# Performance work log

Measured on AMD Instinct MI355X. Metric: run time of the kernel, lower is better.

The kernel has to match this reference:

```python
import jax, jax.numpy as jnp
import numpy as np

B, T, C, H = 4, 2048, 1024, 16
D = C // H          # head_dim = 64
FF = 2 * C          # ff_mult = 2
EPS = 1e-5


def _layernorm(x, g, b):
    mu = jnp.mean(x, axis=-1, keepdims=True)
    var = jnp.mean((x - mu) ** 2, axis=-1, keepdims=True)
    return (x - mu) * jax.lax.rsqrt(var + EPS) * g + b


def setup_inputs() -> dict:
    key = jax.random.key(0)
    ks = jax.random.split(key, 8)
    x = jax.random.normal(ks[0], (B, T, C), dtype=jnp.float32)
    perm = jax.random.permutation(ks[1], T).astype(jnp.int32)
    s_c = 1.0 / np.sqrt(C)
    s_f = 1.0 / np.sqrt(FF)
    Wqkv = jax.random.normal(ks[2], (C, 3 * C), dtype=jnp.float32) * s_c
    Wproj = jax.random.normal(ks[3], (C, C), dtype=jnp.float32) * s_c
    bproj = jnp.zeros((C,), dtype=jnp.float32)
    ln1_g = jnp.ones((C,), dtype=jnp.float32)
    ln1_b = jnp.zeros((C,), dtype=jnp.float32)
    ln2_g = jnp.ones((C,), dtype=jnp.float32)
    ln2_b = jnp.zeros((C,), dtype=jnp.float32)
    Wff1 = jax.random.normal(ks[4], (C, FF), dtype=jnp.float32) * s_c
    bff1 = jnp.zeros((FF,), dtype=jnp.float32)
    Wff2 = jax.random.normal(ks[5], (FF, C), dtype=jnp.float32) * s_f
    bff2 = jnp.zeros((C,), dtype=jnp.float32)
    return {"x": x, "perm": perm, "Wqkv": Wqkv, "Wproj": Wproj, "bproj": bproj,
            "ln1_g": ln1_g, "ln1_b": ln1_b, "ln2_g": ln2_g, "ln2_b": ln2_b,
            "Wff1": Wff1, "bff1": bff1, "Wff2": Wff2, "bff2": bff2}


def reference(x, perm, Wqkv, Wproj, bproj, ln1_g, ln1_b, ln2_g, ln2_b,
              Wff1, bff1, Wff2, bff2):
    # --- attention branch ---
    h = _layernorm(x, ln1_g, ln1_b)                       # [B,T,C]
    qkv = (h @ Wqkv).reshape(B, T, 3, H, D)
    q, k, v = qkv[:, :, 0], qkv[:, :, 1], qkv[:, :, 2]    # [B,T,H,D]
    # random-permuted causal additive mask: masked = ~tril[:, perm]
    rows = jnp.arange(T)[:, None]
    masked = perm[None, :] > rows                          # [T,T] bool
    bias = jnp.where(masked, -jnp.inf, 0.0).astype(x.dtype)
    scale = 1.0 / np.sqrt(D)
    scores = jnp.einsum('bqhd,bkhd->bhqk', q, k) * scale + bias
    attn = jax.nn.softmax(scores, axis=-1)                 # [B,H,T,T]
    y = jnp.einsum('bhqk,bkhd->bqhd', attn, v).reshape(B, T, C)
    x = x + y @ Wproj + bproj
    # --- MLP branch ---
    h2 = _layernorm(x, ln2_g, ln2_b)
    ff = jax.nn.gelu(h2 @ Wff1 + bff1, approximate=False) @ Wff2 + bff2
    return x + ff
```

## Files before the change

kernel.cpp:

```cpp
#include <hip/hip_runtime.h>
#include <math.h>

#define Bb 4
#define Tt 2048
#define Cc 1024
#define Hh 16
#define Dd 64
#define FFf 2048
#define Mrows (Bb*Tt)

typedef _Float16 f16;
typedef _Float16 half8 __attribute__((ext_vector_type(8)));
typedef _Float16 half4 __attribute__((ext_vector_type(4)));
typedef _Float16 half2 __attribute__((ext_vector_type(2)));
typedef float floatx4 __attribute__((ext_vector_type(4)));
typedef float floatx16 __attribute__((ext_vector_type(16)));

#define MFMA16(a,b,c)    __builtin_amdgcn_mfma_f32_16x16x32_f16(a,b,c,0,0,0)
#define MFMA16K16(a,b,c) __builtin_amdgcn_mfma_f32_16x16x16f16(a,b,c,0,0,0)
#define MFMA32(a,b,c)    __builtin_amdgcn_mfma_f32_32x32x16_f16(a,b,c,0,0,0)

__device__ __forceinline__ void g2l16(const void* g, void* l) {
  __builtin_amdgcn_global_load_lds((__attribute__((address_space(1))) void*)(g),
                                   (__attribute__((address_space(3))) void*)(l),
                                   16, 0, 0);
}

__global__ __launch_bounds__(256) void wt_ln_kernel(
    const float* __restrict__ Wqkv, const float* __restrict__ Wproj,
    const float* __restrict__ Wff1, const float* __restrict__ Wff2,
    f16* __restrict__ WqkvT, f16* __restrict__ WprojT,
    f16* __restrict__ Wff1T, f16* __restrict__ Wff2T,
    const float* __restrict__ x, const float* __restrict__ gam,
    const float* __restrict__ bet, f16* __restrict__ lnout,
    const int* __restrict__ perm, int* __restrict__ inv) {
  const int tid = threadIdx.x;
  if (blockIdx.x >= 16384) {
    #pragma unroll
    for (int i = tid; i < Tt; i += 256) inv[perm[i]] = i;
    return;
  }
  if (blockIdx.x < 8192) {
    __shared__ float tile[32][33];
    int idx = blockIdx.x;
    const float* W; f16* WT; int K, N, n0, k0;
    if (idx < 3072)      { W = Wqkv;  WT = WqkvT;  K = Cc;  N = 3*Cc; n0 = (idx % 96)*32; k0 = (idx / 96)*32; }
    else if (idx < 4096) { idx -= 3072; W = Wproj; WT = WprojT; K = Cc;  N = Cc;  n0 = (idx % 32)*32; k0 = (idx / 32)*32; }
    else if (idx < 6144) { idx -= 4096; W = Wff1;  WT = Wff1T;  K = Cc;  N = FFf; n0 = (idx % 64)*32; k0 = (idx / 64)*32; }
    else                 { idx -= 6144; W = Wff2;  WT = Wff2T;  K = FFf; N = Cc;  n0 = (idx % 32)*32; k0 = (idx / 32)*32; }
    const int tx = tid & 31, ty = tid >> 5;
    #pragma unroll
    for (int i = 0; i < 4; i++)
      tile[ty + 8*i][tx] = W[(size_t)(k0 + ty + 8*i) * N + n0 + tx];
    __syncthreads();
    #pragma unroll
    for (int i = 0; i < 4; i++)
      WT[(size_t)(n0 + ty + 8*i) * K + k0 + tx] = (f16)tile[tx][ty + 8*i];
  } else {
    const int row = blockIdx.x - 8192;
    const float4 v = ((const float4*)(x + (size_t)row * Cc))[tid];
    float s  = v.x + v.y + v.z + v.w;
    float ss = v.x*v.x + v.y*v.y + v.z*v.z + v.w*v.w;
    #pragma unroll
    for (int o = 32; o >= 1; o >>= 1) { s += __shfl_xor(s, o); ss += __shfl_xor(ss, o); }
    __shared__ float ps[4], pss[4];
    if ((tid & 63) == 0) { ps[tid >> 6] = s; pss[tid >> 6] = ss; }
    __syncthreads();
    s  = ps[0] + ps[1] + ps[2] + ps[3];
    ss = pss[0] + pss[1] + pss[2] + pss[3];
    const float mu   = s * (1.0f / Cc);
    const float rstd = rsqrtf(ss * (1.0f / Cc) - mu * mu + 1e-5f);
    const float4 g4 = ((const float4*)gam)[tid];
    const float4 b4 = ((const float4*)bet)[tid];
    half4 o;
    o[0] = (f16)((v.x - mu) * rstd * g4.x + b4.x);
    o[1] = (f16)((v.y - mu) * rstd * g4.y + b4.y);
    o[2] = (f16)((v.z - mu) * rstd * g4.z + b4.z);
    o[3] = (f16)((v.w - mu) * rstd * g4.w + b4.w);
    ((half4*)(lnout + (size_t)row * Cc))[tid] = o;
  }
}

__global__ __launch_bounds__(256) void ln_kernel(const float* __restrict__ x,
                                                 const float* __restrict__ gam,
                                                 const float* __restrict__ bet,
                                                 f16* __restrict__ out) {
  const int row = blockIdx.x;
  const int tid = threadIdx.x;
  const float4 v = ((const float4*)(x + (size_t)row * Cc))[tid];
  float s  = v.x + v.y + v.z + v.w;
  float ss = v.x*v.x + v.y*v.y + v.z*v.z + v.w*v.w;
  #pragma unroll
  for (int o = 32; o >= 1; o >>= 1) { s += __shfl_xor(s, o); ss += __shfl_xor(ss, o); }
  __shared__ float ps[4], pss[4];
  if ((tid & 63) == 0) { ps[tid >> 6] = s; pss[tid >> 6] = ss; }
  __syncthreads();
  s  = ps[0] + ps[1] + ps[2] + ps[3];
  ss = pss[0] + pss[1] + pss[2] + pss[3];
  const float mu   = s * (1.0f / Cc);
  const float rstd = rsqrtf(ss * (1.0f / Cc) - mu * mu + 1e-5f);
  const float4 g4 = ((const float4*)gam)[tid];
  const float4 b4 = ((const float4*)bet)[tid];
  half4 o;
  o[0] = (f16)((v.x - mu) * rstd * g4.x + b4.x);
  o[1] = (f16)((v.y - mu) * rstd * g4.y + b4.y);
  o[2] = (f16)((v.z - mu) * rstd * g4.z + b4.z);
  o[3] = (f16)((v.w - mu) * rstd * g4.w + b4.w);
  ((half4*)(out + (size_t)row * Cc))[tid] = o;
}

template <int MODE>
__device__ __forceinline__ void gemm_epilogue_tile(
    const floatx16& a, int rowBase, int col, int khalf,
    const float* __restrict__ resid, const float* __restrict__ bias,
    float* __restrict__ outF, f16* __restrict__ outH,
    f16* __restrict__ outQ, f16* __restrict__ outK, f16* __restrict__ outV) {
  if (MODE == 0) {
    const int s = col >> 10;
    const int hh = (col >> 6) & 15;
    const int d = col & 63;
    #pragma unroll
    for (int g = 0; g < 4; g++) {
      const int row0 = rowBase + 4*khalf + 8*g;
      const int bI = row0 >> 11;
      const int t0 = row0 & 2047;
      if (s == 2) {
        const size_t addr = (((size_t)(bI*Hh + hh)) * Dd + d) * Tt +
                            (t0 & ~63) + ((t0 >> 2) & 3)*16 + ((t0 >> 4) & 3)*4;
        half4 o;
        #pragma unroll
        for (int r = 0; r < 4; r++) o[r] = (f16)a[g*4 + r];
        *(half4*)&outV[addr] = o;
      } else {
        f16* dst = (s == 0) ? outQ : outK;
        const float sc = (s == 0) ? 0.18033688f : 1.0f;
        #pragma unroll
        for (int r = 0; r < 4; r++)
          dst[(((size_t)(bI*Hh + hh)) * Tt + t0 + r) * Dd + d] = (f16)(a[g*4 + r] * sc);
      }
    }
  } else {
    #pragma unroll
    for (int g = 0; g < 4; g++) {
      #pragma unroll
      for (int r = 0; r < 4; r++) {
        const int row = rowBase + 4*khalf + 8*g + r;
        const float vv = a[g*4 + r];
        if (MODE == 1) {
          const size_t ad = (size_t)row * Cc + col;
          outF[ad] = vv + resid[ad] + bias[col];
        } else if (MODE == 2) {
          const float t = vv + bias[col];
          const float gl = 0.5f * t * (1.0f + erff(t * 0.70710678118654752f));
          outH[(size_t)row * FFf + col] = (f16)gl;
        } else {
          const size_t ad = (size_t)row * Cc + col;
          outF[ad] = vv + bias[col] + resid[ad];
        }
      }
    }
  }
}

template <int MODE>
__global__ __launch_bounds__(256, 4) void gemm_kernel(
    const f16* __restrict__ A, const f16* __restrict__ Bt, const int Kdim,
    const float* __restrict__ resid, const float* __restrict__ bias,
    float* __restrict__ outF, f16* __restrict__ outH,
    f16* __restrict__ outQ, f16* __restrict__ outK, f16* __restrict__ outV,
    const int* __restrict__ inv) {
  __shared__ f16 As[128 * 64];
  __shared__ f16 Bs[128 * 64];
  const int tid = threadIdx.x;
  const int lane = tid & 63;
  const int w = tid >> 6;
  const int wr = w >> 1, wc = w & 1;

  const int fid = blockIdx.y * gridDim.x + blockIdx.x;
  const int xcd = fid & 7;
  const int s = fid >> 3;
  const int r = s & 63;
  const int bm = xcd * 8 + (r >> 3);
  const int bn = (s >> 6) * 8 + (r & 7);

  floatx16 acc[2][2] = {};

  const int srow = lane >> 3;
  const int scol = ((lane & 7) ^ srow) * 8;
  size_t aRow[4];
  {
    const int r0 = bm*128 + w*32 + srow;
    if (MODE == 0 && bn >= 8) {
      const int bI = r0 >> 11;
      const int t0 = r0 & 2047;
      #pragma unroll
      for (int c = 0; c < 4; c++)
        aRow[c] = (size_t)(bI*Tt + inv[t0 + c*8]) * Kdim + scol;
    } else {
      #pragma unroll
      for (int c = 0; c < 4; c++)
        aRow[c] = (size_t)(r0 + c*8) * Kdim + scol;
    }
  }
  const size_t bBase = (size_t)(bn*128 + w*32 + srow) * Kdim + scol;

  const int m0 = wr*64 + (lane & 31);
  const int n0 = wc*64 + (lane & 31);
  const int khalf = lane >> 5;
  const int mx = (lane & 7);

  for (int ks = 0; ks < Kdim; ks += 64) {
    __syncthreads();
    #pragma unroll
    for (int c = 0; c < 4; c++) {
      g2l16(A  + aRow[c] + ks, &As[(w*32 + c*8) * 64]);
      g2l16(Bt + bBase + (size_t)(c*8)*Kdim + ks, &Bs[(w*32 + c*8) * 64]);
    }
    __syncthreads();
    #pragma unroll
    for (int kk = 0; kk < 4; kk++) {
      const int kg = kk*2 + khalf;
      half8 aF[2], bF[2];
      aF[0] = *(const half8*)&As[(m0     ) * 64 + ((kg ^ mx) * 8)];
      aF[1] = *(const half8*)&As[(m0 + 32) * 64 + ((kg ^ mx) * 8)];
      bF[0] = *(const half8*)&Bs[(n0     ) * 64 + ((kg ^ mx) * 8)];
      bF[1] = *(const half8*)&Bs[(n0 + 32) * 64 + ((kg ^ mx) * 8)];
      acc[0][0] = MFMA32(aF[0], bF[0], acc[0][0]);
      acc[0][1] = MFMA32(aF[0], bF[1], acc[0][1]);
      acc[1][0] = MFMA32(aF[1], bF[0], acc[1][0]);
      acc[1][1] = MFMA32(aF[1], bF[1], acc[1][1]);
    }
  }

  #pragma unroll
  for (int mi = 0; mi < 2; mi++)
    #pragma unroll
    for (int ni = 0; ni < 2; ni++)
      gemm_epilogue_tile<MODE>(acc[mi][ni], bm*128 + wr*64 + mi*32,
                               bn*128 + wc*64 + ni*32 + (lane & 31), khalf,
                               resid, bias, outF, outH, outQ, outK, outV);
}

__global__ __launch_bounds__(512, 4) void attn_kernel(
    const f16* __restrict__ Q, const f16* __restrict__ Kg,
    const f16* __restrict__ Vtp, f16* __restrict__ Y) {
  __shared__ f16 Ks[64 * 64];
  __shared__ f16 Vs[64 * 64];

  const int tid = threadIdx.x;
  const int lane = tid & 63;
  const int w = tid >> 6;
  const int low = lane & 15;
  const int quad = lane >> 4;
  const int bh = blockIdx.x;
  const int y = blockIdx.y;
  const int b = bh >> 4, h = bh & 15;

  const half4 ones4 = {(f16)1.f, (f16)1.f, (f16)1.f, (f16)1.f};
  const int gd = ((lane & 7) ^ (lane >> 3)) * 8;
  const int krow = lane >> 3;

  for (int pi = 0; pi < 2; pi++) {
    const int tile = (pi == 0) ? y : 15 - y;
    const int q0 = tile * 128;

    half8 qF[2];
    {
      const size_t base = ((size_t)bh * Tt + q0 + w*16) * Dd;
      #pragma unroll
      for (int kc = 0; kc < 2; kc++)
        qF[kc] = *(const half8*)(Q + base + (size_t)low * Dd + kc*32 + quad*8);
    }

    floatx4 O[4] = {};
    floatx4 Ol = {};
    const int nkb = (q0 >> 6) + 2;

    for (int kt = 0; kt < nkb; kt++) {
      const int kbase = kt * 64;
      __syncthreads();
      {
        const size_t kgBase = ((size_t)bh * Tt + kbase) * Dd;
        const size_t vgBase = ((size_t)bh * Dd) * Tt + kbase;
        g2l16(Kg  + kgBase + (size_t)(w*8 + krow) * Dd + gd, &Ks[w * 512]);
        g2l16(Vtp + vgBase + (size_t)(w*8 + krow) * Tt + gd, &Vs[w * 512]);
      }
      __syncthreads();

      floatx4 S[4] = {};
      #pragma unroll
      for (int kc = 0; kc < 2; kc++) {
        #pragma unroll
        for (int ki = 0; ki < 4; ki++) {
          const int key = ki*16 + low;
          const half8 kf = *(const half8*)&Ks[key * 64 + (((kc*4 + quad) ^ (lane & 7)) * 8)];
          S[ki] = MFMA16(kf, qF[kc], S[ki]);
        }
      }

      half4 pF[4];
      const bool needmask = (kbase + 63 > q0 + w*16);
      if (needmask) {
        const int qrow = q0 + w*16 + low;
        #pragma unroll
        for (int ki = 0; ki < 4; ki++) {
          const floatx4 sv = S[ki];
          const int kj = kbase + ki*16 + quad*4;
          const float p0 = (kj + 0 > qrow) ? 0.f : __builtin_amdgcn_exp2f(sv[0]);
          const float p1 = (kj + 1 > qrow) ? 0.f : __builtin_amdgcn_exp2f(sv[1]);
          const float p2 = (kj + 2 > qrow) ? 0.f : __builtin_amdgcn_exp2f(sv[2]);
          const float p3 = (kj + 3 > qrow) ? 0.f : __builtin_amdgcn_exp2f(sv[3]);
          const half2 lo = __builtin_bit_cast(half2, __builtin_amdgcn_cvt_pkrtz(p0, p1));
          const half2 hi = __builtin_bit_cast(half2, __builtin_amdgcn_cvt_pkrtz(p2, p3));
          pF[ki] = __builtin_shufflevector(lo, hi, 0, 1, 2, 3);
        }
      } else {
        #pragma unroll
        for (int ki = 0; ki < 4; ki++) {
          const floatx4 sv = S[ki];
          const float p0 = __builtin_amdgcn_exp2f(sv[0]);
          const float p1 = __builtin_amdgcn_exp2f(sv[1]);
          const float p2 = __builtin_amdgcn_exp2f(sv[2]);
          const float p3 = __builtin_amdgcn_exp2f(sv[3]);
          const half2 lo = __builtin_bit_cast(half2, __builtin_amdgcn_cvt_pkrtz(p0, p1));
          const half2 hi = __builtin_bit_cast(half2, __builtin_amdgcn_cvt_pkrtz(p2, p3));
          pF[ki] = __builtin_shufflevector(lo, hi, 0, 1, 2, 3);
        }
      }

      #pragma unroll
      for (int ki2 = 0; ki2 < 2; ki2++) {
        Ol = MFMA16K16(ones4, pF[2*ki2 + 0], Ol);
        Ol = MFMA16K16(ones4, pF[2*ki2 + 1], Ol);
        #pragma unroll
        for (int ni = 0; ni < 4; ni++) {
          const int d = ni*16 + low;
          const half8 v8 = *(const half8*)&Vs[d * 64 + (((quad*2 + ki2) ^ (lane & 7)) * 8)];
          const half4 vfA = __builtin_shufflevector(v8, v8, 0, 1, 2, 3);
          const half4 vfB = __builtin_shufflevector(v8, v8, 4, 5, 6, 7);
          O[ni] = MFMA16K16(vfA, pF[2*ki2 + 0], O[ni]);
          O[ni] = MFMA16K16(vfB, pF[2*ki2 + 1], O[ni]);
        }
      }
    }

    {
      const float linv = 1.0f / Ol[0];
      const int trow = q0 + w*16 + low;
      #pragma unroll
      for (int ni = 0; ni < 4; ni++) {
        half4 o;
        #pragma unroll
        for (int rr = 0; rr < 4; rr++) o[rr] = (f16)(O[ni][rr] * linv);
        *(half4*)&Y[((size_t)(b * Tt + trow)) * Cc + h*64 + ni*16 + quad*4] = o;
      }
    }
  }
}

extern "C" void kernel_launch(void* const* d_in, const int* in_sizes, int n_in,
                              void* d_out, int out_size, void* d_ws, size_t ws_size,
                              hipStream_t stream) {
  const float* x     = (const float*)d_in[0];
  const int*   perm  = (const int*)d_in[1];
  const float* Wqkv  = (const float*)d_in[2];
  const float* Wproj = (const float*)d_in[3];
  const float* bproj = (const float*)d_in[4];
  const float* ln1g  = (const float*)d_in[5];
  const float* ln1b  = (const float*)d_in[6];
  const float* ln2g  = (const float*)d_in[7];
  const float* ln2b  = (const float*)d_in[8];
  const float* Wff1  = (const float*)d_in[9];
  const float* bff1  = (const float*)d_in[10];
  const float* Wff2  = (const float*)d_in[11];
  const float* bff2  = (const float*)d_in[12];
  float* out = (float*)d_out;

  char* ws = (char*)d_ws;
  size_t off = 0;
  auto alloc = [&](size_t bytes) -> void* {
    void* p = ws + off;
    off += (bytes + 255) & ~(size_t)255;
    return p;
  };
  f16*   h1     = (f16*)alloc((size_t)Mrows * Cc * 2);
  f16*   qb     = (f16*)alloc((size_t)Mrows * Cc * 2);
  f16*   kb     = (f16*)alloc((size_t)Mrows * Cc * 2);
  f16*   vtp    = (f16*)alloc((size_t)Mrows * Cc * 2);
  f16*   yb     = (f16*)alloc((size_t)Mrows * Cc * 2);
  float* xa     = (float*)alloc((size_t)Mrows * Cc * 4);
  f16*   h2     = (f16*)alloc((size_t)Mrows * Cc * 2);
  f16*   gb     = (f16*)alloc((size_t)Mrows * FFf * 2);
  f16*   WqkvT  = (f16*)alloc((size_t)3 * Cc * Cc * 2);
  f16*   WprojT = (f16*)alloc((size_t)Cc * Cc * 2);
  f16*   Wff1T  = (f16*)alloc((size_t)FFf * Cc * 2);
  f16*   Wff2T  = (f16*)alloc((size_t)Cc * FFf * 2);
  int*   inv    = (int*)alloc((size_t)Tt * 4);

  wt_ln_kernel<<<16385, 256, 0, stream>>>(Wqkv, Wproj, Wff1, Wff2,
                                          WqkvT, WprojT, Wff1T, Wff2T,
                                          x, ln1g, ln1b, h1, perm, inv);

  gemm_kernel<0><<<dim3(3*Cc/128, Mrows/128), 256, 0, stream>>>(
      h1, WqkvT, Cc, nullptr, nullptr, nullptr, nullptr, qb, kb, vtp, inv);

  attn_kernel<<<dim3(Bb*Hh, Tt/256), 512, 0, stream>>>(qb, kb, vtp, yb);

  gemm_kernel<1><<<dim3(Cc/128, Mrows/128), 256, 0, stream>>>(
      yb, WprojT, Cc, x, bproj, xa, nullptr, nullptr, nullptr, nullptr, nullptr);

  ln_kernel<<<Mrows, 256, 0, stream>>>(xa, ln2g, ln2b, h2);

  gemm_kernel<2><<<dim3(FFf/128, Mrows/128), 256, 0, stream>>>(
      h2, Wff1T, Cc, nullptr, bff1, nullptr, gb, nullptr, nullptr, nullptr, nullptr);

  gemm_kernel<3><<<dim3(Cc/128, Mrows/128), 256, 0, stream>>>(
      gb, Wff2T, FFf, xa, bff2, out, nullptr, nullptr, nullptr, nullptr, nullptr);
}
```

Before: 402.1 us.

## Add double-buffered 256x256-tile GEMM kernel for QKV and FF1 projections

Introduces a new GEMM kernel with 256x256 output tiles, 512 threads, and double-buffered LDS that prefetches the next K-slice via global_load_lds while MFMAs run on the current one, with s_setprio around the MFMA block. The QKV and FF1 GEMMs switch to it, while the old 128-tile kernel stays for the projection and FF2 GEMMs. Larger tiles raise arithmetic intensity and the prefetch overlaps loads with compute. In exchange, fewer blocks run (384 and 256), LDS use reaches 128KB per block, and wave quantization on the CUs may suffer.

```diff
diff --git a/kernel.cpp b/kernel.cpp
--- a/kernel.cpp
+++ b/kernel.cpp
@@ -190,17 +190,9 @@
   size_t aRow[4];
   {
     const int r0 = bm*128 + w*32 + srow;
-    if (MODE == 0 && bn >= 8) {
-      const int bI = r0 >> 11;
-      const int t0 = r0 & 2047;
-      #pragma unroll
-      for (int c = 0; c < 4; c++)
-        aRow[c] = (size_t)(bI*Tt + inv[t0 + c*8]) * Kdim + scol;
-    } else {
-      #pragma unroll
-      for (int c = 0; c < 4; c++)
-        aRow[c] = (size_t)(r0 + c*8) * Kdim + scol;
-    }
+    #pragma unroll
+    for (int c = 0; c < 4; c++)
+      aRow[c] = (size_t)(r0 + c*8) * Kdim + scol;
   }
   const size_t bBase = (size_t)(bn*128 + w*32 + srow) * Kdim + scol;
 
@@ -239,6 +231,107 @@
       gemm_epilogue_tile<MODE>(acc[mi][ni], bm*128 + wr*64 + mi*32,
                                bn*128 + wc*64 + ni*32 + (lane & 31), khalf,
                                resid, bias, outF, outH, outQ, outK, outV);
+}
+
+template <int MODE>
+__global__ __launch_bounds__(512, 2) void gemm256_kernel(
+    const f16* __restrict__ A, const f16* __restrict__ Bt, const int Kdim,
+    const float* __restrict__ bias,
+    float* __restrict__ outF, f16* __restrict__ outH,
+    f16* __restrict__ outQ, f16* __restrict__ outK, f16* __restrict__ outV,
+    const int* __restrict__ inv) {
+  __shared__ f16 As[2][256 * 64];
+  __shared__ f16 Bs[2][256 * 64];
+  const int tid = threadIdx.x;
+  const int lane = tid & 63;
+  const int w = tid >> 6;
+  const int wr = w >> 2, wc = w & 3;
+
+  const int fid = blockIdx.y * gridDim.x + blockIdx.x;
+  const int xcd = fid & 7;
+  const int s = fid >> 3;
+  const int bm = xcd * 4 + (s & 3);
+  const int bn = s >> 2;
+
+  floatx16 acc[4][2] = {};
+
+  const int srow = lane >> 3;
+  const int scol = ((lane & 7) ^ srow) * 8;
+  size_t aRow[4], bRow[4];
+  {
+    const int r0 = bm*256 + w*32 + srow;
+    if (MODE == 0 && bn >= 4) {
+      const int bI = r0 >> 11;
+      const int t0 = r0 & 2047;
+      #pragma unroll
+      for (int c = 0; c < 4; c++)
+        aRow[c] = (size_t)(bI*Tt + inv[t0 + c*8]) * Kdim + scol;
+    } else {
+      #pragma unroll
+      for (int c = 0; c < 4; c++)
+        aRow[c] = (size_t)(r0 + c*8) * Kdim + scol;
+    }
+    const int rb = bn*256 + w*32 + srow;
+    #pragma unroll
+    for (int c = 0; c < 4; c++)
+      bRow[c] = (size_t)(rb + c*8) * Kdim + scol;
+  }
+
+  const int m0 = wr*128 + (lane & 31);
+  const int n0 = wc*64  + (lane & 31);
+  const int khalf = lane >> 5;
+  const int mx = (lane & 7);
+  const int NT = Kdim >> 6;
+
+  #pragma unroll
+  for (int c = 0; c < 4; c++) {
+    g2l16(A  + aRow[c], &As[0][(w*32 + c*8) * 64]);
+    g2l16(Bt + bRow[c], &Bs[0][(w*32 + c*8) * 64]);
+  }
+  asm volatile("s_waitcnt vmcnt(0)" ::: "memory");
+  __builtin_amdgcn_s_barrier();
+
+  for (int t = 0; t < NT; ++t) {
+    const int cur = t & 1;
+    #pragma unroll
+    for (int kk = 0; kk < 4; ++kk) {
+      const int kg = kk*2 + khalf;
+      half8 aF[4], bF[2];
+      #pragma unroll
+      for (int mi = 0; mi < 4; mi++)
+        aF[mi] = *(const half8*)&As[cur][(m0 + mi*32) * 64 + ((kg ^ mx) * 8)];
+      #pragma unroll
+      for (int ni = 0; ni < 2; ni++)
+        bF[ni] = *(const half8*)&Bs[cur][(n0 + ni*32) * 64 + ((kg ^ mx) * 8)];
+      if (kk == 0 && t + 1 < NT) {
+        const size_t ks = (size_t)(t + 1) * 64;
+        #pragma unroll
+        for (int c = 0; c < 4; c++) {
+          g2l16(A  + aRow[c] + ks, &As[cur ^ 1][(w*32 + c*8) * 64]);
+          g2l16(Bt + bRow[c] + ks, &Bs[cur ^ 1][(w*32 + c*8) * 64]);
+        }
+      }
+      __builtin_amdgcn_s_barrier();
+      __builtin_amdgcn_s_setprio(1);
+      #pragma unroll
+      for (int mi = 0; mi < 4; mi++) {
+        acc[mi][0] = MFMA32(aF[mi], bF[0], acc[mi][0]);
+        acc[mi][1] = MFMA32(aF[mi], bF[1], acc[mi][1]);
+      }
+      __builtin_amdgcn_s_setprio(0);
+      if (kk == 3)
+        asm volatile("s_waitcnt vmcnt(0)" ::: "memory");
+      __builtin_amdgcn_s_barrier();
+    }
+  }
+
+  #pragma unroll
+  for (int mi = 0; mi < 4; mi++)
+    #pragma unroll
+    for (int ni = 0; ni < 2; ni++)
+      gemm_epilogue_tile<MODE>(acc[mi][ni], bm*256 + wr*128 + mi*32,
+                               bn*256 + wc*64 + ni*32 + (lane & 31), khalf,
+                               nullptr, bias, outF, outH, outQ, outK, outV);
 }
 
 __global__ __launch_bounds__(512, 4) void attn_kernel(
@@ -401,8 +494,8 @@
                                           WqkvT, WprojT, Wff1T, Wff2T,
                                           x, ln1g, ln1b, h1, perm, inv);
 
-  gemm_kernel<0><<<dim3(3*Cc/128, Mrows/128), 256, 0, stream>>>(
-      h1, WqkvT, Cc, nullptr, nullptr, nullptr, nullptr, qb, kb, vtp, inv);
+  gemm256_kernel<0><<<dim3(12, 32), 512, 0, stream>>>(
+      h1, WqkvT, Cc, nullptr, nullptr, nullptr, qb, kb, vtp, inv);
 
   attn_kernel<<<dim3(Bb*Hh, Tt/256), 512, 0, stream>>>(qb, kb, vtp, yb);
 
@@ -411,8 +504,8 @@
 
   ln_kernel<<<Mrows, 256, 0, stream>>>(xa, ln2g, ln2b, h2);
 
-  gemm_kernel<2><<<dim3(FFf/128, Mrows/128), 256, 0, stream>>>(
-      h2, Wff1T, Cc, nullptr, bff1, nullptr, gb, nullptr, nullptr, nullptr, nullptr);
+  gemm256_kernel<2><<<dim3(8, 32), 512, 0, stream>>>(
+      h2, Wff1T, Cc, bff1, nullptr, gb, nullptr, nullptr, nullptr, nullptr);
 
   gemm_kernel<3><<<dim3(Cc/128, Mrows/128), 256, 0, stream>>>(
       gb, Wff2T, FFf, xa, bff2, out, nullptr, nullptr, nullptr, nullptr, nullptr);
```

New measurement: 419.0 us. 1.04x slower.
